# Optimization experiments

Hardware: AMD Instinct MI355X
Metric: run time of the kernel (lower is better)

Reference implementation:

```python
import jax, jax.numpy as jnp
import numpy as np
from jax import lax

FILTERS = 32
NEIGH = 5


def _conv3d_same(x, w, b=None):
    out = lax.conv_general_dilated(x, w, window_strides=(1, 1, 1), padding='SAME',
                                   dimension_numbers=('NCDHW', 'OIDHW', 'NCDHW'))
    return out if b is None else out + b[None, :, None, None, None]


def _avgpool2(x):
    s = lax.reduce_window(x, 0.0, lax.add, (1, 1, 2, 2, 2), (1, 1, 2, 2, 2), 'VALID')
    return s * 0.125


def _grid_sample_3d(vol, grid):
    # trilinear, zeros padding, align_corners=False (torch defaults)
    Din, Hin, Win = vol.shape
    ix = ((grid[..., 0] + 1.0) * Win - 1.0) * 0.5
    iy = ((grid[..., 1] + 1.0) * Hin - 1.0) * 0.5
    iz = ((grid[..., 2] + 1.0) * Din - 1.0) * 0.5
    x0f, y0f, z0f = jnp.floor(ix), jnp.floor(iy), jnp.floor(iz)
    wx, wy, wz = ix - x0f, iy - y0f, iz - z0f
    x0 = x0f.astype(jnp.int32); y0 = y0f.astype(jnp.int32); z0 = z0f.astype(jnp.int32)

    def tap(z, y, x, w):
        valid = (z >= 0) & (z < Din) & (y >= 0) & (y < Hin) & (x >= 0) & (x < Win)
        v = vol[jnp.clip(z, 0, Din - 1), jnp.clip(y, 0, Hin - 1), jnp.clip(x, 0, Win - 1)]
        return jnp.where(valid, v, 0.0) * w

    return (tap(z0,     y0,     x0,     (1 - wz) * (1 - wy) * (1 - wx))
          + tap(z0,     y0,     x0 + 1, (1 - wz) * (1 - wy) * wx)
          + tap(z0,     y0 + 1, x0,     (1 - wz) * wy * (1 - wx))
          + tap(z0,     y0 + 1, x0 + 1, (1 - wz) * wy * wx)
          + tap(z0 + 1, y0,     x0,     wz * (1 - wy) * (1 - wx))
          + tap(z0 + 1, y0,     x0 + 1, wz * (1 - wy) * wx)
          + tap(z0 + 1, y0 + 1, x0,     wz * wy * (1 - wx))
          + tap(z0 + 1, y0 + 1, x0 + 1, wz * wy * wx))


def _forward(x, conv_w, conv_b, gaus_w):
    D = _avgpool2(_conv3d_same(x, conv_w, conv_b))           # (B, c, h, w, d)
    p = _conv3d_same(D, gaus_w)                              # (B, c, h, w, d)
    B, c, h, w, d = D.shape
    # normalized coordinate field P: (3, h, w, d)
    P = jnp.stack([
        jnp.broadcast_to(jnp.arange(h, dtype=D.dtype)[:, None, None] / (h - 1), (h, w, d)),
        jnp.broadcast_to(jnp.arange(w, dtype=D.dtype)[None, :, None] / (w - 1), (h, w, d)),
        jnp.broadcast_to(jnp.arange(d, dtype=D.dtype)[None, None, :] / (d - 1), (h, w, d)),
    ])
    # (B, 3, c, h, w, d) -> (3B, c, h, w, d) for a single batched gaussian conv
    D_mul = (P[None, :, None] * D[:, None]).reshape(3 * B, c, h, w, d)
    allf = _conv3d_same(D_mul, gaus_w).reshape(B, 3, c, h, w, d)
    filt = jnp.clip(allf / (p[:, None] + 1e-6) * 2.0 - 1.0, -1.0, 1.0)
    grids = jnp.transpose(filt, (0, 2, 3, 4, 5, 1))          # (B, c, h, w, d, 3)
    Bx, Cx, Hx, Wx, Dx = x.shape
    vols = x.reshape(B * c, Hx, Wx, Dx)
    g = grids.reshape(B * c, h, w, d, 3)
    y = jax.vmap(_grid_sample_3d)(vols, g).reshape(B, c, h, w, d)
    return y, D, jnp.mean(grids, axis=1)


def setup_inputs() -> dict:
    key = jax.random.key(0)
    k1, k2, k3 = jax.random.split(key, 3)
    x = jax.random.normal(k1, (2, FILTERS, 64, 64, 64), dtype=jnp.float32)
    fan_in = FILTERS * 3 * 3 * 3
    conv_w = (jax.random.normal(k2, (FILTERS, FILTERS, 3, 3, 3), dtype=jnp.float32)
              / np.float32(np.sqrt(fan_in)))
    conv_b = jax.random.normal(k3, (FILTERS,), dtype=jnp.float32) * 0.01
    # fixed gaussian kernel, replicated across in/out channels (as in makegaussian)
    center = NEIGH // 2
    co = np.arange(NEIGH) - center
    zz, yy, xx = np.meshgrid(co, co, co, indexing='ij')
    gk = np.exp(-4.0 * np.log(2.0) * (zz ** 2 + yy ** 2 + xx ** 2) / NEIGH ** 2).astype(np.float32)
    gaus_w = jnp.asarray(np.broadcast_to(gk, (FILTERS, FILTERS, NEIGH, NEIGH, NEIGH)).copy())
    return {"x": x, "conv_w": conv_w, "conv_b": conv_b, "gaus_w": gaus_w}


def reference(x, conv_w, conv_b, gaus_w):
    return _forward(x, conv_w, conv_b, gaus_w)
```

## Files before the change

### kernel.cpp

```cpp
#include <hip/hip_runtime.h>
#include <hip/hip_bf16.h>


#define XN 64
#define DN 32
#define C  32
#define XVOL (XN * XN * XN)
#define DVOL (DN * DN * DN)

typedef __attribute__((ext_vector_type(8))) short short8v;
typedef __attribute__((ext_vector_type(4))) float float4v;

struct __attribute__((packed, aligned(4))) f4u { float4v v; };
struct __attribute__((packed, aligned(4))) s8u { short8v v; };

static __device__ __forceinline__ short f2bf(float f) {
    union { float f; unsigned u; } v; v.f = f;
    unsigned r = (v.u + 0x7fffu + ((v.u >> 16) & 1u)) >> 16;
    return (short)r;
}

static __device__ __forceinline__ unsigned pk2(float a, float b) {
    __hip_bfloat162 h = __float22bfloat162_rn(float2{a, b});
    union { __hip_bfloat162 h2; unsigned u; } cv; cv.h2 = h;
    return cv.u;
}

static __device__ __forceinline__ float w4val(const float* __restrict__ conv_w,
                                              int ic, int u, int oc) {
    int uz = u >> 4, uy = (u >> 2) & 3, ux = u & 3;
    float s = 0.f;
    #pragma unroll
    for (int sz = 0; sz < 2; ++sz) {
        int tz = uz - sz; if (tz < 0 || tz > 2) continue;
        #pragma unroll
        for (int sy = 0; sy < 2; ++sy) {
            int ty = uy - sy; if (ty < 0 || ty > 2) continue;
            #pragma unroll
            for (int sx = 0; sx < 2; ++sx) {
                int tx = ux - sx; if (tx < 0 || tx > 2) continue;
                s += conv_w[(oc * C + ic) * 27 + tz * 9 + ty * 3 + tx];
            }
        }
    }
    return 0.125f * s;
}

__global__ __launch_bounds__(256) void k_prep(const float* __restrict__ conv_w,
                                              const float* __restrict__ conv_b,
                                              unsigned short* __restrict__ wfrag,
                                              float* __restrict__ wsum) {
    int bid = blockIdx.x;
    int tid = threadIdx.x;
    if (bid < 256) {
        int i = bid * 256 + tid;
        int e = i & 7;
        int l = (i >> 3) & 63;
        int sf = i >> 9;
        int f = sf & 1, step = sf >> 1;
        int oc = f * 16 + (l & 15);
        int k = step * 32 + ((l >> 4) * 8 + e);
        float v = w4val(conv_w, k >> 6, k & 63, oc);
        wfrag[i] = (unsigned short)f2bf(v);
        if (i == 0) {
            float s = 0.f;
            for (int o = 0; o < C; ++o) s += conv_b[o];
            wsum[2048] = s;
        }
    } else {
        int i2 = (bid - 256) * 256 + tid;
        int oc = tid & 31;
        int kk = i2 >> 5;
        float v = w4val(conv_w, kk >> 6, kk & 63, oc);
        v += __shfl_xor(v, 1, 64);
        v += __shfl_xor(v, 2, 64);
        v += __shfl_xor(v, 4, 64);
        v += __shfl_xor(v, 8, 64);
        v += __shfl_xor(v, 16, 64);
        if (oc == 0) wsum[kk] = v;
    }
}

#define NSTG (6 * 6 * 34)
#define TILEF (6 * 6 * 36)

__global__ __launch_bounds__(256) void k_conv_mfma(
        const float* __restrict__ x, const unsigned short* __restrict__ wfrag,
        const float* __restrict__ wsum, const float* __restrict__ bias,
        float* __restrict__ Dout, float* __restrict__ Dsum) {
    __shared__ float tilepair[2][2 * TILEF];
    __shared__ char wbuf[2 * 8320];
    __shared__ float wsb[2][132];
    int tid = threadIdx.x;

    int bid = blockIdx.x;
    int wid = (bid & 7) * 128 + (bid >> 3);
    int xt = wid & 1;
    int yt = (wid >> 1) & 15;
    int zt = (wid >> 5) & 15;
    int b  = wid >> 9;
    int w = tid >> 6, lane = tid & 63;
    int col = lane & 15, g = lane >> 4;
    int wpz = w >> 1, wpy = w & 1;
    int pz = zt * 2 + wpz, py = yt * 2 + wpy, px = xt * 16 + col;

    const float* xb = x + (size_t)b * C * XVOL;
    const char* wfb = (const char*)wfrag;
    int wsdst = (tid >> 6) * 1040 + (tid & 63) * 16;

    int gz0 = zt * 4 - 1, gy0 = yt * 4 - 1, gx0 = xt * 32 - 1;
    int  soff[5], sdst[5];
    bool sval[5], swr[5];
    #pragma unroll
    for (int it = 0; it < 5; ++it) {
        int i = tid + it * 256;
        int lx = i % 34; int r = i / 34; int ly = r % 6; int lz = r / 6;
        int gz = gz0 + lz, gy = gy0 + ly, gx = gx0 + lx;
        bool inr = i < NSTG;
        swr[it]  = inr;
        sval[it] = inr && (unsigned)gz < XN && (unsigned)gy < XN && (unsigned)gx < XN;
        soff[it] = ((gz & 63) * XN + (gy & 63)) * XN + (gx & 63);
        sdst[it] = inr ? (lz * 6 + ly) * 36 + lx : 0;
    }

    int base_g = ((2 * wpz + (g >> 1)) * 6 + 2 * wpy + (g & 1) * 2) * 36 + 2 * col;

    float4v acc0 = {0.f, 0.f, 0.f, 0.f};
    float4v acc1 = {0.f, 0.f, 0.f, 0.f};
    float4v dpv = {0.f, 0.f, 0.f, 0.f};
    float svA[10], svB[10];
    short8v sg0, sg1;
    float wv;

#define TLOADP(SV, p) do {                                                   \
    const float* xp0 = xb + (size_t)(2 * (p)) * XVOL;                        \
    _Pragma("unroll")                                                        \
    for (int it = 0; it < 5; ++it)                                           \
        SV[it] = sval[it] ? xp0[soff[it]] : 0.f;                             \
    const float* xp1 = xp0 + XVOL;                                           \
    _Pragma("unroll")                                                        \
    for (int it = 0; it < 5; ++it)                                           \
        SV[5 + it] = sval[it] ? xp1[soff[it]] : 0.f;                         \
} while (0)

#define TWRITEP(bf, SV) do {                                                 \
    float* d0 = tilepair[bf];                                                \
    _Pragma("unroll")                                                        \
    for (int it = 0; it < 5; ++it)                                           \
        if (swr[it]) d0[sdst[it]] = SV[it];                                  \
    float* d1 = tilepair[bf] + TILEF;                                        \
    _Pragma("unroll")                                                        \
    for (int it = 0; it < 5; ++it)                                           \
        if (swr[it]) d1[sdst[it]] = SV[5 + it];                              \
} while (0)

#define WLOAD(p) do {                                                        \
    const char* wp = wfb + (size_t)(p) * 8192 + tid * 16;                    \
    sg0 = ((const s8u*)(wp))->v;                                             \
    sg1 = ((const s8u*)(wp + 4096))->v;                                      \
    wv = (tid < 128) ? wsum[(p) * 128 + tid] : 0.f;                          \
} while (0)

#define WWRITE(bf) do {                                                      \
    *(short8v*)(wbuf + (bf) * 8320 + wsdst) = sg0;                           \
    *(short8v*)(wbuf + (bf) * 8320 + 4160 + wsdst) = sg1;                    \
    if (tid < 128) wsb[bf][tid] = wv;                                        \
} while (0)

#define COMPT(bf, icL) do {                                                  \
    const float* t = tilepair[bf] + (icL) * TILEF;                           \
    _Pragma("unroll")                                                        \
    for (int h5 = 0; h5 < 2; ++h5) {                                         \
        int off0 = base_g + h5 * 432;                                        \
        float2 v01 = *(const float2*)&t[off0];                               \
        float2 v23 = *(const float2*)&t[off0 + 2];                           \
        float2 v45 = *(const float2*)&t[off0 + 36];                          \
        float2 v67 = *(const float2*)&t[off0 + 38];                          \
        float4v r0 = {v01.x, v01.y, v23.x, v23.y};                           \
        float4v r1 = {v45.x, v45.y, v67.x, v67.y};                           \
        const float4v wlo = *(const float4v*)&wsb[bf][((icL) * 2 + h5) * 32 + g * 8];     \
        const float4v whi = *(const float4v*)&wsb[bf][((icL) * 2 + h5) * 32 + g * 8 + 4]; \
        dpv += wlo * r0;                                                     \
        dpv += whi * r1;                                                     \
        union { short8v s; unsigned u[4]; } Bv;                              \
        Bv.u[0] = pk2(r0[0], r0[1]); Bv.u[1] = pk2(r0[2], r0[3]);            \
        Bv.u[2] = pk2(r1[0], r1[1]); Bv.u[3] = pk2(r1[2], r1[3]);            \
        const char* wl = wbuf + (bf) * 8320 + (icL) * 4160 + lane * 16;      \
        short8v w0 = *(const short8v*)(wl + (h5 * 2) * 1040);                \
        short8v w1 = *(const short8v*)(wl + (h5 * 2 + 1) * 1040);            \
        acc0 = __builtin_amdgcn_mfma_f32_16x16x32_bf16(w0, Bv.s, acc0, 0, 0, 0); \
        acc1 = __builtin_amdgcn_mfma_f32_16x16x32_bf16(w1, Bv.s, acc1, 0, 0, 0); \
    }                                                                        \
} while (0)

    WLOAD(0);
    WWRITE(0);
    TLOADP(svA, 0);
    TWRITEP(0, svA);
    TLOADP(svB, 1);
    __syncthreads();

    #pragma unroll 2
    for (int p = 0; p < 16; ++p) {
        int buf = p & 1;
        if (p + 2 < 16) {
            if (buf == 0) TLOADP(svA, p + 2); else TLOADP(svB, p + 2);
        }
        if (p + 1 < 16) WLOAD(p + 1);
        COMPT(buf, 0);
        COMPT(buf, 1);
        if (p + 1 < 16) {
            if (buf == 0) TWRITEP(1, svB); else TWRITEP(0, svA);
            WWRITE(buf ^ 1);
            __syncthreads();
        }
    }

#undef TLOADP
#undef TWRITEP
#undef WLOAD
#undef WWRITE
#undef COMPT

    float dp = (dpv[0] + dpv[1]) + (dpv[2] + dpv[3]);
    dp += __shfl_xor(dp, 16, 64);
    dp += __shfl_xor(dp, 32, 64);

    int sp = pz * (DN * DN) + py * DN + px;
    float4v b0 = *(const float4v*)&bias[g * 4];
    float4v b1 = *(const float4v*)&bias[16 + g * 4];
    #pragma unroll
    for (int r = 0; r < 4; ++r) {
        int oc0 = g * 4 + r;
        int oc1 = 16 + g * 4 + r;
        Dout[(size_t)(b * C + oc0) * DVOL + sp] = acc0[r] + b0[r];
        Dout[(size_t)(b * C + oc1) * DVOL + sp] = acc1[r] + b1[r];
    }
    if (g == 0)
        Dsum[b * DVOL + sp] = dp + wsum[2048];
}

__global__ __launch_bounds__(256) void k_gauss(const float* __restrict__ Dsum,
                                               const float* __restrict__ gaus_w,
                                               float* __restrict__ filt,
                                               float* __restrict__ outg) {
    __shared__ float tg[8 * 12 * 12];
    __shared__ float gk[125];
    int bid = blockIdx.x;
    int xt = bid & 3, yt = (bid >> 2) & 3, zt = (bid >> 4) & 7, b = bid >> 7;
    int tid = threadIdx.x;
    if (tid < 125) gk[tid] = gaus_w[tid];
    const float* Ds = Dsum + b * DVOL;
    for (int i = tid; i < 1152; i += 256) {
        int lx = i % 12; int r = i / 12; int ly = r % 12; int lz = r / 12;
        int gz = zt * 4 - 2 + lz, gy = yt * 8 - 2 + ly, gx = xt * 8 - 2 + lx;
        float v = 0.f;
        if ((unsigned)gz < DN && (unsigned)gy < DN && (unsigned)gx < DN)
            v = Ds[(gz * DN + gy) * DN + gx];
        tg[i] = v;
    }
    __syncthreads();
    int px = tid & 7, py = (tid >> 3) & 7, pz = tid >> 6;
    const float inv31 = 1.f / 31.f;
    float zb = (float)(zt * 4 + pz - 2);
    float yb = (float)(yt * 8 + py - 2);
    float xb = (float)(xt * 8 + px - 2);
    float p = 0.f, a0 = 0.f, a1 = 0.f, a2 = 0.f;
    for (int tz = 0; tz < 5; ++tz)
    for (int ty = 0; ty < 5; ++ty) {
        int base = ((pz + tz) * 12 + py + ty) * 12 + px;
        #pragma unroll
        for (int tx = 0; tx < 5; ++tx) {
            float g = gk[tz * 25 + ty * 5 + tx];
            float v = g * tg[base + tx];
            p += v;
            a0 = fmaf(v, (zb + (float)tz) * inv31, a0);
            a1 = fmaf(v, (yb + (float)ty) * inv31, a1);
            a2 = fmaf(v, (xb + (float)tx) * inv31, a2);
        }
    }
    float denom = p + 1e-6f;
    float f0 = fminf(fmaxf(a0 / denom * 2.f - 1.f, -1.f), 1.f);
    float f1 = fminf(fmaxf(a1 / denom * 2.f - 1.f, -1.f), 1.f);
    float f2 = fminf(fmaxf(a2 / denom * 2.f - 1.f, -1.f), 1.f);
    int sp = ((zt * 4 + pz) * DN + yt * 8 + py) * DN + xt * 8 + px;
    filt[(b * 3 + 0) * DVOL + sp] = f0;
    filt[(b * 3 + 1) * DVOL + sp] = f1;
    filt[(b * 3 + 2) * DVOL + sp] = f2;
    outg[(size_t)(b * DVOL + sp) * 3 + 0] = f0;
    outg[(size_t)(b * DVOL + sp) * 3 + 1] = f1;
    outg[(size_t)(b * DVOL + sp) * 3 + 2] = f2;
}

__global__ __launch_bounds__(128) void k_sample(const float* __restrict__ x,
                                                const float* __restrict__ filt,
                                                float* __restrict__ y) {
    int bid = blockIdx.x;
    int wid = (bid & 7) * 1024 + (bid >> 3);
    int xt = wid & 1;
    int yt = (wid >> 1) & 7;
    int zt = (wid >> 4) & 15;
    int cgrp = (wid >> 8) & 15;
    int b  = wid >> 12;
    int tid = threadIdx.x;
    int px = tid & 15, py = (tid >> 4) & 3, pz = tid >> 6;
    int sp = ((zt * 2 + pz) * DN + yt * 4 + py) * DN + xt * 16 + px;
    const float* fb = filt + b * 3 * DVOL;
    float g0 = fb[sp], g1 = fb[DVOL + sp], g2 = fb[2 * DVOL + sp];

    float ix = ((g0 + 1.0f) * (float)XN - 1.0f) * 0.5f;
    float iy = ((g1 + 1.0f) * (float)XN - 1.0f) * 0.5f;
    float iz = ((g2 + 1.0f) * (float)XN - 1.0f) * 0.5f;
    float x0f = floorf(ix), y0f = floorf(iy), z0f = floorf(iz);
    float wx = ix - x0f, wyf = iy - y0f, wz = iz - z0f;
    int x0 = (int)x0f, y0i = (int)y0f, z0 = (int)z0f;

    int offs[8];
    float wts[8];
    #pragma unroll
    for (int t = 0; t < 8; ++t) {
        int dz = t >> 2, dy = (t >> 1) & 1, dx = t & 1;
        int zc = z0 + dz, yc = y0i + dy, xc = x0 + dx;
        bool valid = (unsigned)zc < (unsigned)XN && (unsigned)yc < (unsigned)XN &&
                     (unsigned)xc < (unsigned)XN;
        int zcl = min(max(zc, 0), XN - 1);
        int ycl = min(max(yc, 0), XN - 1);
        int xcl = min(max(xc, 0), XN - 1);
        offs[t] = zcl * (XN * XN) + ycl * XN + xcl;
        float w = (dz ? wz : 1.f - wz) * (dy ? wyf : 1.f - wyf) * (dx ? wx : 1.f - wx);
        wts[t] = valid ? w : 0.f;
    }

    const float* xc0 = x + (size_t)(b * C + cgrp * 2) * XVOL;
    float t0[8], t1[8];
    #pragma unroll
    for (int k = 0; k < 8; ++k) t0[k] = xc0[offs[k]];
    #pragma unroll
    for (int k = 0; k < 8; ++k) t1[k] = xc0[XVOL + offs[k]];

    float a0 = 0.f, a1 = 0.f;
    #pragma unroll
    for (int k = 0; k < 8; ++k) a0 = fmaf(wts[k], t0[k], a0);
    #pragma unroll
    for (int k = 0; k < 8; ++k) a1 = fmaf(wts[k], t1[k], a1);
    y[(size_t)(b * C + cgrp * 2 + 0) * DVOL + sp] = a0;
    y[(size_t)(b * C + cgrp * 2 + 1) * DVOL + sp] = a1;
}

extern "C" void kernel_launch(void* const* d_in, const int* in_sizes, int n_in,
                              void* d_out, int out_size, void* d_ws, size_t ws_size,
                              hipStream_t stream) {
    const float* x      = (const float*)d_in[0];
    const float* conv_w = (const float*)d_in[1];
    const float* conv_b = (const float*)d_in[2];
    const float* gaus_w = (const float*)d_in[3];

    float* out = (float*)d_out;
    float* y_out = out;
    float* D_out = out + (size_t)2097152;
    float* g_out = out + (size_t)4194304;

    float* ws   = (float*)d_ws;
    float* Dsum = ws;
    float* filt = ws + 65536;
    float* wsum = ws + 262144;
    unsigned short* wfrag = (unsigned short*)(ws + 264256);

    k_prep<<<dim3(512), dim3(256), 0, stream>>>(conv_w, conv_b, wfrag, wsum);
    k_conv_mfma<<<dim3(1024), dim3(256), 0, stream>>>(x, wfrag, wsum, conv_b,
                                                      D_out, Dsum);
    k_gauss<<<dim3(256), dim3(256), 0, stream>>>(Dsum, gaus_w, filt, g_out);
    k_sample<<<dim3(8192), dim3(128), 0, stream>>>(x, filt, y_out);
    (void)in_sizes; (void)n_in; (void)out_size; (void)ws_size;
}
```

Baseline: 97.10 us.

## Restructure conv pipeline to write next tile before compute with single register stage

The conv MFMA main loop now writes the already-loaded next input tile and weights into the alternate shared buffer at the top of each iteration, then issues the global loads for the stage after that, then computes. The two register staging arrays become one, and the unroll-2 pragma is dropped. This frees registers and lets the global loads run underneath the compute. The risk is that the loads now have to land before the next iteration's writes at its top, so there is less time to hide their latency than before.

```diff
diff --git a/kernel.cpp b/kernel.cpp
--- a/kernel.cpp
+++ b/kernel.cpp
@@ -88,7 +88,7 @@
         const float* __restrict__ x, const unsigned short* __restrict__ wfrag,
         const float* __restrict__ wsum, const float* __restrict__ bias,
         float* __restrict__ Dout, float* __restrict__ Dsum) {
-    __shared__ float tilepair[2][2 * TILEF];
+    __shared__ float tile[2][2 * TILEF];
     __shared__ char wbuf[2 * 8320];
     __shared__ float wsb[2][132];
     int tid = threadIdx.x;
@@ -128,7 +128,7 @@
     float4v acc0 = {0.f, 0.f, 0.f, 0.f};
     float4v acc1 = {0.f, 0.f, 0.f, 0.f};
     float4v dpv = {0.f, 0.f, 0.f, 0.f};
-    float svA[10], svB[10];
+    float svT[10];
     short8v sg0, sg1;
     float wv;
 
@@ -144,11 +144,11 @@
 } while (0)
 
 #define TWRITEP(bf, SV) do {                                                 \
-    float* d0 = tilepair[bf];                                                \
+    float* d0 = tile[bf];                                                    \
     _Pragma("unroll")                                                        \
     for (int it = 0; it < 5; ++it)                                           \
         if (swr[it]) d0[sdst[it]] = SV[it];                                  \
-    float* d1 = tilepair[bf] + TILEF;                                        \
+    float* d1 = tile[bf] + TILEF;                                            \
     _Pragma("unroll")                                                        \
     for (int it = 0; it < 5; ++it)                                           \
         if (swr[it]) d1[sdst[it]] = SV[5 + it];                              \
@@ -168,7 +168,7 @@
 } while (0)
 
 #define COMPT(bf, icL) do {                                                  \
-    const float* t = tilepair[bf] + (icL) * TILEF;                           \
+    const float* t = tile[bf] + (icL) * TILEF;                               \
     _Pragma("unroll")                                                        \
     for (int h5 = 0; h5 < 2; ++h5) {                                         \
         int off0 = base_g + h5 * 432;                                        \
@@ -195,25 +195,24 @@
 
     WLOAD(0);
     WWRITE(0);
-    TLOADP(svA, 0);
-    TWRITEP(0, svA);
-    TLOADP(svB, 1);
+    TLOADP(svT, 0);
+    TWRITEP(0, svT);
+    TLOADP(svT, 1);
+    WLOAD(1);
     __syncthreads();
 
-    #pragma unroll 2
     for (int p = 0; p < 16; ++p) {
-        int buf = p & 1;
+        if (p > 0) __syncthreads();
+        if (p + 1 < 16) {
+            TWRITEP((p + 1) & 1, svT);
+            WWRITE((p + 1) & 1);
+        }
         if (p + 2 < 16) {
-            if (buf == 0) TLOADP(svA, p + 2); else TLOADP(svB, p + 2);
-        }
-        if (p + 1 < 16) WLOAD(p + 1);
-        COMPT(buf, 0);
-        COMPT(buf, 1);
-        if (p + 1 < 16) {
-            if (buf == 0) TWRITEP(1, svB); else TWRITEP(0, svA);
-            WWRITE(buf ^ 1);
-            __syncthreads();
-        }
+            TLOADP(svT, p + 2);
+            WLOAD(p + 2);
+        }
+        COMPT(p & 1, 0);
+        COMPT(p & 1, 1);
     }
 
 #undef TLOADP
```

Result: faster. 84.45 us (-13.0%).
